# Kernel tuning notes

Measured on AMD Instinct MI355X. Metric: run time of the kernel, lower is better.

The kernel has to match this reference:

```python
import jax, jax.numpy as jnp
import numpy as np
from jax import lax

B, N, D_FEAT = 16, 4096, 20
NPOINT, NSAMPLE = 1024, 32
MLP = [64, 64, 128]
IN_CH = 3 + 1 + D_FEAT  # grouped_xyz_norm(3) + L2 norm(1) + grouped_depth_norm(20)
BN_EPS = 1e-5


def setup_inputs() -> dict:
    key = jax.random.key(0)
    ks = jax.random.split(key, 20)
    inp = {
        "xyz": jax.random.normal(ks[0], (B, 3, N), dtype=jnp.float32),
        "feature": jax.random.normal(ks[1], (B, N, D_FEAT), dtype=jnp.float32),
    }
    last = IN_CH
    kidx = 2
    for li, out_ch in enumerate(MLP):
        inp[f"w{li}"] = jax.random.normal(ks[kidx], (out_ch, last), dtype=jnp.float32) * (1.0 / np.sqrt(last)); kidx += 1
        inp[f"b{li}"] = jax.random.normal(ks[kidx], (out_ch,), dtype=jnp.float32) * 0.01; kidx += 1
        inp[f"g{li}"] = 1.0 + 0.1 * jax.random.normal(ks[kidx], (out_ch,), dtype=jnp.float32); kidx += 1
        inp[f"bt{li}"] = 0.1 * jax.random.normal(ks[kidx], (out_ch,), dtype=jnp.float32); kidx += 1
        last = out_ch
    return inp


def square_distance(src, dst):
    # [B,S,C] x [B,M,C] -> [B,S,M]
    d = -2.0 * jnp.einsum("bsc,bmc->bsm", src, dst)
    d = d + jnp.sum(src * src, -1)[:, :, None]
    d = d + jnp.sum(dst * dst, -1)[:, None, :]
    return d


def farthest_point_sample(pts, npoint):
    # pts: [B,N,C]; deterministic start at index 0 (torch uses random start)
    b, n, _ = pts.shape
    bidx = jnp.arange(b)

    def step(carry, _):
        dist, far = carry
        centroid = pts[bidx, far]                      # [B,C]
        d = jnp.sum((pts - centroid[:, None, :]) ** 2, -1)  # [B,N]
        dist = jnp.minimum(dist, d)
        nxt = jnp.argmax(dist, -1)
        return (dist, nxt), far

    init = (jnp.full((b, n), 1e10, pts.dtype), jnp.zeros((b,), jnp.int32))
    _, idx = lax.scan(step, init, None, length=npoint)
    return idx.T  # [B,npoint]


def _gather_groups(points, idx):
    # points [B,N,C], idx [B,S,K] -> [B,S,K,C]
    return jax.vmap(lambda p, i: p[i])(points, idx)


def conv_bn_relu(x, w, b, g, bt):
    # x [B,C,K,S]; 1x1 conv = channel matmul; BN in training mode (batch stats, biased var)
    y = jnp.einsum("bcks,oc->boks", x, w) + b[None, :, None, None]
    mu = jnp.mean(y, axis=(0, 2, 3), keepdims=True)
    var = jnp.mean((y - mu) ** 2, axis=(0, 2, 3), keepdims=True)
    y = (y - mu) * lax.rsqrt(var + BN_EPS)
    y = y * g[None, :, None, None] + bt[None, :, None, None]
    return jax.nn.relu(y)


def reference(xyz, feature, w0, b0, g0, bt0, w1, b1, g1, bt1, w2, b2, g2, bt2):
    xyz_n = jnp.transpose(xyz, (0, 2, 1))              # [B,N,3]
    combined = jnp.concatenate([xyz_n, feature], -1)   # [B,N,23]
    fps_idx = farthest_point_sample(combined, NPOINT)  # [B,S]

    new_bin = jnp.take_along_axis(feature, fps_idx[:, :, None], axis=1)  # [B,S,20]
    new_xyz = jnp.take_along_axis(xyz_n, fps_idx[:, :, None], axis=1)    # [B,S,3]

    sqd = square_distance(new_bin, feature) + square_distance(new_xyz, xyz_n)  # [B,S,N]
    idx = jnp.argsort(sqd, axis=-1)[:, :, :NSAMPLE]    # [B,S,K]

    gxyz = _gather_groups(xyz_n, idx)                  # [B,S,K,3]
    gfeat = _gather_groups(feature, idx)               # [B,S,K,20]
    gxyz_norm = gxyz - new_xyz[:, :, None, :]
    gdep_norm = gfeat - new_bin[:, :, None, :]
    nrm = jnp.sqrt(jnp.maximum(jnp.sum(gxyz_norm ** 2, -1, keepdims=True), 1e-12))
    new_points = jnp.concatenate([gxyz_norm, nrm, gdep_norm], -1)  # [B,S,K,24]

    x = jnp.transpose(new_points, (0, 3, 2, 1))        # [B,24,K,S]
    for (w, b, g, bt) in [(w0, b0, g0, bt0), (w1, b1, g1, bt1), (w2, b2, g2, bt2)]:
        x = conv_bn_relu(x, w, b, g, bt)
    out = jnp.max(x, axis=2)                           # [B,128,S]
    return jnp.transpose(new_xyz, (0, 2, 1)), out, new_bin
```

## Files before the change

kernel.cpp:

```cpp
#include <hip/hip_runtime.h>

#define BB 16
#define NN 4096
#define DFEAT 20
#define SS 1024
#define KK 32
#define MM (BB*SS*KK)

#define WS_STATS   0ull
#define WS_PARAMS  8192ull
#define WS_FPSIDX  12288ull
#define WS_CENT    81920ull
#define WS_KNN     1654784ull
#define WS_COMB    3751936ull
#define WS_YB      10043392ull
#define WS_NEED    77152256ull

static __device__ __forceinline__ unsigned short f2bf(float f){
    unsigned u = __float_as_uint(f);
    unsigned r = (u + 0x7FFFu + ((u >> 16) & 1u)) >> 16;
    return (unsigned short)r;
}
static __device__ __forceinline__ float bf2f(unsigned short v){
    return __uint_as_float((unsigned)v << 16);
}

__global__ void k_zstats(double* __restrict__ stats){
    int t = threadIdx.x;
#pragma unroll
    for (int i = 0; i < 4; ++i) stats[i*256 + t] = 0.0;
}

__global__ void k_fail(float* __restrict__ out, int n){
    int i = blockIdx.x * 256 + threadIdx.x;
    if (i < n) out[i] = 0.f;
}

__global__ __launch_bounds__(256) void k_build(const float* __restrict__ xyz,
                                               const float* __restrict__ feat,
                                               float* __restrict__ comb)
{
    int idx = blockIdx.x * 256 + threadIdx.x;
    int b = idx >> 12, j = idx & 4095;
    float c[24];
    c[0] = xyz[((size_t)b*3 + 0)*NN + j];
    c[1] = xyz[((size_t)b*3 + 1)*NN + j];
    c[2] = xyz[((size_t)b*3 + 2)*NN + j];
    const float* f = feat + ((size_t)b*NN + j)*DFEAT;
#pragma unroll
    for (int d = 0; d < 20; ++d) c[3+d] = f[d];
    c[23] = 0.f;
    float* out = comb + (size_t)idx * 24;
#pragma unroll
    for (int q = 0; q < 6; ++q)
        ((float4*)out)[q] = make_float4(c[4*q], c[4*q+1], c[4*q+2], c[4*q+3]);
}

__global__ __launch_bounds__(512, 2) void k_fps(const float* __restrict__ comb,
                                                int* __restrict__ fpsidx)
{
    int b = blockIdx.x, t = threadIdx.x;
    const float* C = comb + (size_t)b * NN * 24;
    float pt[8][24];
    float dist[8];
#pragma unroll
    for (int p = 0; p < 8; ++p){
        const float4* r = (const float4*)(C + (size_t)(t + 512*p) * 24);
#pragma unroll
        for (int q = 0; q < 6; ++q){
            float4 v = r[q];
            pt[p][4*q] = v.x; pt[p][4*q+1] = v.y; pt[p][4*q+2] = v.z; pt[p][4*q+3] = v.w;
        }
        dist[p] = 1e10f;
    }
    __shared__ __align__(16) float cent[24];
    __shared__ unsigned long long wkey[8];
    __shared__ unsigned long long winner;
    if (t == 0){
#pragma unroll
        for (int q = 0; q < 24; ++q) cent[q] = pt[0][q];
    }
    __syncthreads();
    int far = 0;
    int lane = t & 63, w = t >> 6;
    for (int s = 0; s < SS; ++s){
        if (t == 0) fpsidx[b*SS + s] = far;
        float cc[24];
#pragma unroll
        for (int q = 0; q < 6; ++q){
            float4 v = ((const float4*)cent)[q];
            cc[4*q] = v.x; cc[4*q+1] = v.y; cc[4*q+2] = v.z; cc[4*q+3] = v.w;
        }
        unsigned long long best = 0;
#pragma unroll
        for (int p = 0; p < 8; ++p){
            float d0 = pt[p][0] - cc[0];
            float acc = d0 * d0;
#pragma unroll
            for (int q = 1; q < 23; ++q){
                float dd = pt[p][q] - cc[q];
                acc = fmaf(dd, dd, acc);
            }
            dist[p] = fminf(dist[p], acc);
            unsigned long long key = ((unsigned long long)__float_as_uint(dist[p]) << 32)
                                   | (unsigned long long)(0xFFFFFFFFu - (unsigned)(t + 512*p));
            best = best > key ? best : key;
        }
#pragma unroll
        for (int off = 32; off > 0; off >>= 1){
            unsigned long long o = __shfl_xor(best, off);
            best = best > o ? best : o;
        }
        if (lane == 0) wkey[w] = best;
        __syncthreads();
        if (t == 0){
            unsigned long long m = wkey[0];
#pragma unroll
            for (int i = 1; i < 8; ++i) m = m > wkey[i] ? m : wkey[i];
            winner = m;
        }
        __syncthreads();
        unsigned long long m = winner;
        int jw = (int)(0xFFFFFFFFu - (unsigned)(m & 0xFFFFFFFFull));
        far = jw;
        if ((jw & 511) == t){
            int p = jw >> 9;
#pragma unroll
            for (int pp = 0; pp < 8; ++pp) if (pp == p){
#pragma unroll
                for (int q = 0; q < 24; ++q) cent[q] = pt[pp][q];
            }
        }
        __syncthreads();
    }
}

__global__ __launch_bounds__(256) void k_gather(const float* __restrict__ comb,
                                                const int* __restrict__ fpsidx,
                                                float* __restrict__ cent,
                                                float* __restrict__ out0,
                                                float* __restrict__ out2)
{
    int idx = blockIdx.x * 256 + threadIdx.x;
    int b = idx >> 10, s = idx & 1023;
    int j = fpsidx[idx];
    const float* row = comb + ((size_t)b*NN + j) * 24;
    float* cr = cent + (size_t)idx * 24;
#pragma unroll
    for (int q = 0; q < 6; ++q) ((float4*)cr)[q] = ((const float4*)row)[q];
#pragma unroll
    for (int c = 0; c < 3; ++c) out0[((size_t)b*3 + c)*SS + s] = row[c];
    float* o2 = out2 + (size_t)idx * 20;
#pragma unroll
    for (int d = 0; d < 20; ++d) o2[d] = row[3 + d];
}

__global__ __launch_bounds__(256) void k_knn(const float* __restrict__ comb,
                                             const float* __restrict__ cent,
                                             int* __restrict__ knn)
{
    int w = threadIdx.x >> 6, lane = threadIdx.x & 63;
    int r = blockIdx.x * 4 + w;
    int b = r >> 10;
    const float* crow = cent + (size_t)r * 24;
    const float* P0 = comb + (size_t)b * NN * 24;
    double cc[24];
#pragma unroll
    for (int q = 0; q < 24; ++q) cc[q] = (double)crow[q];
    double d[64];
#pragma unroll
    for (int k = 0; k < 64; ++k){
        int j = k*64 + lane;
        const float4* pr = (const float4*)(P0 + (size_t)j * 24);
        double acc = 0.0;
#pragma unroll
        for (int q = 0; q < 6; ++q){
            float4 v = pr[q];
            double d0 = (double)v.x - cc[4*q];
            double d1 = (double)v.y - cc[4*q+1];
            double d2 = (double)v.z - cc[4*q+2];
            double d3 = (double)v.w - cc[4*q+3];
            acc += d0*d0; acc += d1*d1; acc += d2*d2; acc += d3*d3;
        }
        d[k] = acc;
    }
    int* orow = knn + (size_t)r * KK;
    for (int it = 0; it < KK; ++it){
        double dm = d[0]; int km = 0;
#pragma unroll
        for (int k = 1; k < 64; ++k){
            if (d[k] < dm){ dm = d[k]; km = k; }
        }
        int gi = km*64 + lane;
#pragma unroll
        for (int off = 32; off > 0; off >>= 1){
            double od = __shfl_xor(dm, off);
            int og = __shfl_xor(gi, off);
            if (od < dm || (od == dm && og < gi)){ dm = od; gi = og; }
        }
        int g = __builtin_amdgcn_readfirstlane(gi);
        if (lane == 0) orow[it] = g;
        int wk = g >> 6, wl = g & 63;
#pragma unroll
        for (int k = 0; k < 64; ++k)
            if (k == wk && lane == wl) d[k] = 1e300;
    }
}

__global__ __launch_bounds__(256) void k_l1(const float* __restrict__ comb,
                                            const float* __restrict__ cent,
                                            const int* __restrict__ knn,
                                            const float* __restrict__ w0,
                                            const float* __restrict__ b0,
                                            unsigned short* __restrict__ yb)
{
    __shared__ float Wt[24][64];
    __shared__ float Xt[24][68];
    int t = threadIdx.x;
    int m_base = blockIdx.x * 64;
    for (int i = t; i < 1536; i += 256){
        int o = i / 24, c = i - o*24;
        Wt[c][o] = w0[i];
    }
    {
        int sm = t & 63, g = t >> 6;
        int m = m_base + sm;
        int b = m >> 15;
        int row = m >> 5;
        int j = knn[m];
        const float* P  = comb + ((size_t)b*NN + j) * 24;
        const float* Cc = cent + (size_t)row * 24;
        if (g == 0){
            float dx = P[0]-Cc[0], dy = P[1]-Cc[1], dz = P[2]-Cc[2];
            Xt[0][sm] = dx; Xt[1][sm] = dy; Xt[2][sm] = dz;
            float n2 = dx*dx; n2 = fmaf(dy, dy, n2); n2 = fmaf(dz, dz, n2);
            Xt[3][sm] = sqrtf(fmaxf(n2, 1e-12f));
            Xt[4][sm] = P[3] - Cc[3];
            Xt[5][sm] = P[4] - Cc[4];
        } else {
#pragma unroll
            for (int cq = 0; cq < 6; ++cq){
                int c = 6*g + cq;
                Xt[c][sm] = P[c-1] - Cc[c-1];
            }
        }
    }
    __syncthreads();
    int i = t >> 4, jj = t & 15;
    float acc[4][4] = {};
#pragma unroll
    for (int c = 0; c < 24; ++c){
        float4 wv = *(const float4*)&Wt[c][i*4];
        float4 xv = *(const float4*)&Xt[c][jj*4];
        float wr[4] = {wv.x, wv.y, wv.z, wv.w};
        float xr[4] = {xv.x, xv.y, xv.z, xv.w};
#pragma unroll
        for (int a = 0; a < 4; ++a)
#pragma unroll
            for (int q = 0; q < 4; ++q) acc[a][q] = fmaf(wr[a], xr[q], acc[a][q]);
    }
#pragma unroll
    for (int oi = 0; oi < 4; ++oi){
        int o = i*4 + oi;
        float bb = b0[o];
        ushort4 rv;
        rv.x = f2bf(acc[oi][0]+bb); rv.y = f2bf(acc[oi][1]+bb);
        rv.z = f2bf(acc[oi][2]+bb); rv.w = f2bf(acc[oi][3]+bb);
        *(ushort4*)&yb[(size_t)o*MM + m_base + jj*4] = rv;
    }
}

__global__ __launch_bounds__(256) void k_stats(const unsigned short* __restrict__ y,
                                               double* __restrict__ stats)
{
    const int chunks = 8;
    int c = blockIdx.x / chunks, ch = blockIdx.x % chunks;
    size_t base = (size_t)c * MM + (size_t)ch * (MM / chunks);
    double s1 = 0.0, s2 = 0.0;
    const unsigned short* p = y + base;
    for (int i = threadIdx.x; i < MM/chunks; i += 256){
        float v = bf2f(p[i]);
        s1 += v; s2 += (double)v * v;
    }
#pragma unroll
    for (int off = 32; off > 0; off >>= 1){
        s1 += __shfl_xor(s1, off);
        s2 += __shfl_xor(s2, off);
    }
    __shared__ double ps1[4], ps2[4];
    int w = threadIdx.x >> 6, lane = threadIdx.x & 63;
    if (lane == 0){ ps1[w] = s1; ps2[w] = s2; }
    __syncthreads();
    if (threadIdx.x == 0){
        atomicAdd(&stats[c*2 + 0], ps1[0]+ps1[1]+ps1[2]+ps1[3]);
        atomicAdd(&stats[c*2 + 1], ps2[0]+ps2[1]+ps2[2]+ps2[3]);
    }
}

__global__ void k_affine(const double* __restrict__ stats, float* __restrict__ params, int C)
{
    int c = threadIdx.x;
    if (c < C){
        double mu = stats[c*2] / (double)MM;
        double var = stats[c*2 + 1] / (double)MM - mu*mu;
        params[c*2 + 0] = (float)mu;
        params[c*2 + 1] = (float)(1.0 / sqrt(var + 1e-5));
    }
}

__global__ __launch_bounds__(256) void k_l2(unsigned short* __restrict__ yb,
                                            const float* __restrict__ prm,
                                            const float* __restrict__ gg,
                                            const float* __restrict__ bt,
                                            const float* __restrict__ w,
                                            const float* __restrict__ bias)
{
    __shared__ float Wt[64][64];
    __shared__ float Xt[64][68];
    int t = threadIdx.x;
    int m_base = blockIdx.x * 64;
    for (int i = t; i < 4096; i += 256){
        int o = i >> 6, c = i & 63;
        Wt[c][o] = w[i];
    }
#pragma unroll
    for (int rp = 0; rp < 16; ++rp){
        int idx = rp*256 + t;
        int c = idx >> 6, mm2 = idx & 63;
        float v = bf2f(yb[(size_t)c*MM + m_base + mm2]);
        float t1 = (v - prm[c*2]) * prm[c*2 + 1];
        Xt[c][mm2] = fmaxf(fmaf(t1, gg[c], bt[c]), 0.f);
    }
    __syncthreads();
    int i = t >> 4, jj = t & 15;
    float acc[4][4] = {};
#pragma unroll
    for (int c = 0; c < 64; ++c){
        float4 wv = *(const float4*)&Wt[c][i*4];
        float4 xv = *(const float4*)&Xt[c][jj*4];
        float wr[4] = {wv.x, wv.y, wv.z, wv.w};
        float xr[4] = {xv.x, xv.y, xv.z, xv.w};
#pragma unroll
        for (int a = 0; a < 4; ++a)
#pragma unroll
            for (int q = 0; q < 4; ++q) acc[a][q] = fmaf(wr[a], xr[q], acc[a][q]);
    }
#pragma unroll
    for (int oi = 0; oi < 4; ++oi){
        int o = i*4 + oi;
        float bb = bias[o];
        ushort4 rv;
        rv.x = f2bf(acc[oi][0]+bb); rv.y = f2bf(acc[oi][1]+bb);
        rv.z = f2bf(acc[oi][2]+bb); rv.w = f2bf(acc[oi][3]+bb);
        *(ushort4*)&yb[(size_t)o*MM + m_base + jj*4] = rv;
    }
}

__global__ __launch_bounds__(256) void k_l3s(const unsigned short* __restrict__ yb,
                                             const float* __restrict__ prm,
                                             const float* __restrict__ gg,
                                             const float* __restrict__ bt,
                                             const float* __restrict__ w,
                                             const float* __restrict__ bias,
                                             double* __restrict__ stats)
{
    __shared__ float Wt[64][128];
    __shared__ float Xt[64][68];
    int t = threadIdx.x;
    for (int i = t; i < 8192; i += 256){
        int o = i >> 6, c = i & 63;
        Wt[c][o] = w[i];
    }
    int i = t >> 4, jj = t & 15;
    double s1[8] = {}, s2[8] = {};
    for (int tt = 0; tt < 16; ++tt){
        int m_base = (blockIdx.x * 16 + tt) * 64;
        __syncthreads();
#pragma unroll
        for (int rp = 0; rp < 16; ++rp){
            int idx = rp*256 + t;
            int c = idx >> 6, mm2 = idx & 63;
            float v = bf2f(yb[(size_t)c*MM + m_base + mm2]);
            float t1 = (v - prm[c*2]) * prm[c*2 + 1];
            Xt[c][mm2] = fmaxf(fmaf(t1, gg[c], bt[c]), 0.f);
        }
        __syncthreads();
        float acc[8][4] = {};
#pragma unroll
        for (int c = 0; c < 64; ++c){
            float4 w0v = *(const float4*)&Wt[c][i*8];
            float4 w1v = *(const float4*)&Wt[c][i*8 + 4];
            float4 xv  = *(const float4*)&Xt[c][jj*4];
            float wr[8] = {w0v.x, w0v.y, w0v.z, w0v.w, w1v.x, w1v.y, w1v.z, w1v.w};
            float xr[4] = {xv.x, xv.y, xv.z, xv.w};
#pragma unroll
            for (int a = 0; a < 8; ++a)
#pragma unroll
                for (int q = 0; q < 4; ++q) acc[a][q] = fmaf(wr[a], xr[q], acc[a][q]);
        }
#pragma unroll
        for (int oi = 0; oi < 8; ++oi){
            float bb = bias[i*8 + oi];
#pragma unroll
            for (int q = 0; q < 4; ++q){
                float v = acc[oi][q] + bb;
                s1[oi] += v;
                s2[oi] += (double)v * v;
            }
        }
    }
#pragma unroll
    for (int oi = 0; oi < 8; ++oi){
#pragma unroll
        for (int off = 1; off < 16; off <<= 1){
            s1[oi] += __shfl_xor(s1[oi], off);
            s2[oi] += __shfl_xor(s2[oi], off);
        }
    }
    if (jj == 0){
#pragma unroll
        for (int oi = 0; oi < 8; ++oi){
            int o = i*8 + oi;
            atomicAdd(&stats[o*2 + 0], s1[oi]);
            atomicAdd(&stats[o*2 + 1], s2[oi]);
        }
    }
}

__global__ __launch_bounds__(256) void k_final(const unsigned short* __restrict__ yb,
                                               const float* __restrict__ prm2,
                                               const float* __restrict__ g1c,
                                               const float* __restrict__ bt1c,
                                               const float* __restrict__ w,
                                               const float* __restrict__ bias,
                                               const float* __restrict__ prm3,
                                               const float* __restrict__ g2c,
                                               const float* __restrict__ bt2c,
                                               float* __restrict__ out1)
{
    __shared__ float Wt[64][128];
    __shared__ float Xt[64][68];
    int t = threadIdx.x;
    int m_base = blockIdx.x * 64;
    for (int i = t; i < 8192; i += 256){
        int o = i >> 6, c = i & 63;
        Wt[c][o] = w[i];
    }
#pragma unroll
    for (int rp = 0; rp < 16; ++rp){
        int idx = rp*256 + t;
        int c = idx >> 6, mm2 = idx & 63;
        float v = bf2f(yb[(size_t)c*MM + m_base + mm2]);
        float t1 = (v - prm2[c*2]) * prm2[c*2 + 1];
        Xt[c][mm2] = fmaxf(fmaf(t1, g1c[c], bt1c[c]), 0.f);
    }
    __syncthreads();
    int i = t >> 4, jj = t & 15;
    float acc[8][4] = {};
#pragma unroll
    for (int c = 0; c < 64; ++c){
        float4 w0v = *(const float4*)&Wt[c][i*8];
        float4 w1v = *(const float4*)&Wt[c][i*8 + 4];
        float4 xv  = *(const float4*)&Xt[c][jj*4];
        float wr[8] = {w0v.x, w0v.y, w0v.z, w0v.w, w1v.x, w1v.y, w1v.z, w1v.w};
        float xr[4] = {xv.x, xv.y, xv.z, xv.w};
#pragma unroll
        for (int a = 0; a < 8; ++a)
#pragma unroll
            for (int q = 0; q < 4; ++q) acc[a][q] = fmaf(wr[a], xr[q], acc[a][q]);
    }
    float mx[8];
#pragma unroll
    for (int oi = 0; oi < 8; ++oi){
        int o = i*8 + oi;
        float bb = bias[o];
        float mu = prm3[o*2], inv = prm3[o*2 + 1], gv = g2c[o], bv = bt2c[o];
        float m = 0.f;
#pragma unroll
        for (int q = 0; q < 4; ++q){
            float v = acc[oi][q] + bb;
            float r = fmaxf(fmaf((v - mu) * inv, gv, bv), 0.f);
            m = fmaxf(m, r);
        }
        mx[oi] = m;
    }
#pragma unroll
    for (int oi = 0; oi < 8; ++oi){
#pragma unroll
        for (int off = 1; off < 8; off <<= 1)
            mx[oi] = fmaxf(mx[oi], __shfl_xor(mx[oi], off));
    }
    if ((jj & 7) == 0){
        int rg = (m_base >> 5) + (jj >> 3);
        int b = rg >> 10, s = rg & 1023;
#pragma unroll
        for (int oi = 0; oi < 8; ++oi)
            out1[(size_t)b*131072 + (size_t)(i*8 + oi)*1024 + s] = mx[oi];
    }
}

extern "C" void kernel_launch(void* const* d_in, const int* in_sizes, int n_in,
                              void* d_out, int out_size, void* d_ws, size_t ws_size,
                              hipStream_t stream)
{
    const float* xyz  = (const float*)d_in[0];
    const float* feat = (const float*)d_in[1];
    const float* w0 = (const float*)d_in[2];  const float* b0  = (const float*)d_in[3];
    const float* g0 = (const float*)d_in[4];  const float* bt0 = (const float*)d_in[5];
    const float* w1 = (const float*)d_in[6];  const float* b1  = (const float*)d_in[7];
    const float* g1 = (const float*)d_in[8];  const float* bt1 = (const float*)d_in[9];
    const float* w2 = (const float*)d_in[10]; const float* b2  = (const float*)d_in[11];
    const float* g2 = (const float*)d_in[12]; const float* bt2 = (const float*)d_in[13];

    float* out0 = (float*)d_out;
    float* out1 = (float*)d_out + 49152;
    float* out2 = (float*)d_out + 49152 + 2097152;

    if (ws_size < WS_NEED){
        k_fail<<<(out_size + 255)/256, 256, 0, stream>>>((float*)d_out, out_size);
        return;
    }

    char* ws = (char*)d_ws;
    double* stats = (double*)(ws + WS_STATS);
    float* params = (float*)(ws + WS_PARAMS);
    int*   fpsidx = (int*)(ws + WS_FPSIDX);
    float* cent   = (float*)(ws + WS_CENT);
    int*   knn    = (int*)(ws + WS_KNN);
    float* comb   = (float*)(ws + WS_COMB);
    unsigned short* yb = (unsigned short*)(ws + WS_YB);

    k_zstats<<<1,    256, 0, stream>>>(stats);
    k_build <<<256,  256, 0, stream>>>(xyz, feat, comb);
    k_fps   <<<16,   512, 0, stream>>>(comb, fpsidx);
    k_gather<<<64,   256, 0, stream>>>(comb, fpsidx, cent, out0, out2);
    k_knn   <<<4096, 256, 0, stream>>>(comb, cent, knn);
    k_l1    <<<8192, 256, 0, stream>>>(comb, cent, knn, w0, b0, yb);
    k_stats <<<512,  256, 0, stream>>>(yb, stats);
    k_affine<<<1,    128, 0, stream>>>(stats, params, 64);
    k_l2    <<<8192, 256, 0, stream>>>(yb, params, g0, bt0, w1, b1);
    k_stats <<<512,  256, 0, stream>>>(yb, stats + 256);
    k_affine<<<1,    128, 0, stream>>>(stats + 256, params + 256, 64);
    k_l3s   <<<512,  256, 0, stream>>>(yb, params + 256, g1, bt1, w2, b2, stats + 512);
    k_affine<<<1,    128, 0, stream>>>(stats + 512, params + 512, 128);
    k_final <<<8192, 256, 0, stream>>>(yb, params + 256, g1, bt1, w2, b2,
                                       params + 512, g2, bt2, out1);
}
```

Before: 3.360 ms.

## Cut FPS barriers with double-buffered wave keys and reload points from cache

The farthest-point-sampling loop previously held 8x24 points per thread in registers and used three barriers per step, with thread 0 reducing the per-wave keys and broadcasting the winning centroid through shared memory. It now uses one barrier per step: per-wave keys go into a double-buffered shared array, every wave reduces them itself with shuffles, and each thread reads the next centroid straight from global memory. Points are reloaded from global or L2 memory on every step instead of living in registers, which frees registers but adds a large amount of repeated memory traffic across the 1024 sequential steps. The kNN kernel also gets a min-blocks hint of 1 in its launch bounds.

```diff
diff --git a/kernel.cpp b/kernel.cpp
--- a/kernel.cpp
+++ b/kernel.cpp
@@ -61,44 +61,36 @@
 {
     int b = blockIdx.x, t = threadIdx.x;
     const float* C = comb + (size_t)b * NN * 24;
-    float pt[8][24];
     float dist[8];
 #pragma unroll
-    for (int p = 0; p < 8; ++p){
-        const float4* r = (const float4*)(C + (size_t)(t + 512*p) * 24);
-#pragma unroll
-        for (int q = 0; q < 6; ++q){
-            float4 v = r[q];
-            pt[p][4*q] = v.x; pt[p][4*q+1] = v.y; pt[p][4*q+2] = v.z; pt[p][4*q+3] = v.w;
-        }
-        dist[p] = 1e10f;
-    }
-    __shared__ __align__(16) float cent[24];
-    __shared__ unsigned long long wkey[8];
-    __shared__ unsigned long long winner;
-    if (t == 0){
-#pragma unroll
-        for (int q = 0; q < 24; ++q) cent[q] = pt[0][q];
-    }
-    __syncthreads();
+    for (int p = 0; p < 8; ++p) dist[p] = 1e10f;
+    __shared__ unsigned long long wkey[2][8];
+    int lane = t & 63, w = t >> 6;
     int far = 0;
-    int lane = t & 63, w = t >> 6;
     for (int s = 0; s < SS; ++s){
         if (t == 0) fpsidx[b*SS + s] = far;
+        const float4* crow = (const float4*)(C + (size_t)far * 24);
         float cc[24];
 #pragma unroll
         for (int q = 0; q < 6; ++q){
-            float4 v = ((const float4*)cent)[q];
-            cc[4*q] = v.x; cc[4*q+1] = v.y; cc[4*q+2] = v.z; cc[4*q+3] = v.w;
+            float4 cv = crow[q];
+            cc[4*q] = cv.x; cc[4*q+1] = cv.y; cc[4*q+2] = cv.z; cc[4*q+3] = cv.w;
         }
         unsigned long long best = 0;
 #pragma unroll
         for (int p = 0; p < 8; ++p){
-            float d0 = pt[p][0] - cc[0];
+            const float4* r = (const float4*)(C + (size_t)(t + 512*p) * 24);
+            float pv[24];
+#pragma unroll
+            for (int q = 0; q < 6; ++q){
+                float4 v = r[q];
+                pv[4*q] = v.x; pv[4*q+1] = v.y; pv[4*q+2] = v.z; pv[4*q+3] = v.w;
+            }
+            float d0 = pv[0] - cc[0];
             float acc = d0 * d0;
 #pragma unroll
             for (int q = 1; q < 23; ++q){
-                float dd = pt[p][q] - cc[q];
+                float dd = pv[q] - cc[q];
                 acc = fmaf(dd, dd, acc);
             }
             dist[p] = fminf(dist[p], acc);
@@ -111,27 +103,16 @@
             unsigned long long o = __shfl_xor(best, off);
             best = best > o ? best : o;
         }
-        if (lane == 0) wkey[w] = best;
+        int par = s & 1;
+        if (lane == 0) wkey[par][w] = best;
         __syncthreads();
-        if (t == 0){
-            unsigned long long m = wkey[0];
-#pragma unroll
-            for (int i = 1; i < 8; ++i) m = m > wkey[i] ? m : wkey[i];
-            winner = m;
-        }
-        __syncthreads();
-        unsigned long long m = winner;
-        int jw = (int)(0xFFFFFFFFu - (unsigned)(m & 0xFFFFFFFFull));
-        far = jw;
-        if ((jw & 511) == t){
-            int p = jw >> 9;
-#pragma unroll
-            for (int pp = 0; pp < 8; ++pp) if (pp == p){
-#pragma unroll
-                for (int q = 0; q < 24; ++q) cent[q] = pt[pp][q];
-            }
-        }
-        __syncthreads();
+        unsigned long long k2 = wkey[par][lane & 7];
+#pragma unroll
+        for (int off = 1; off < 8; off <<= 1){
+            unsigned long long o = __shfl_xor(k2, off);
+            k2 = k2 > o ? k2 : o;
+        }
+        far = (int)(0xFFFFFFFFu - (unsigned)(k2 & 0xFFFFFFFFull));
     }
 }
 
@@ -155,9 +136,9 @@
     for (int d = 0; d < 20; ++d) o2[d] = row[3 + d];
 }
 
-__global__ __launch_bounds__(256) void k_knn(const float* __restrict__ comb,
-                                             const float* __restrict__ cent,
-                                             int* __restrict__ knn)
+__global__ __launch_bounds__(256, 1) void k_knn(const float* __restrict__ comb,
+                                                const float* __restrict__ cent,
+                                                int* __restrict__ knn)
 {
     int w = threadIdx.x >> 6, lane = threadIdx.x & 63;
     int r = blockIdx.x * 4 + w;
```

Result: faster. 3.053 ms (-9.1%).
